# Performance work log

Measured on AMD Instinct MI355X. Metric: run time of the kernel, lower is better.

The kernel has to match this reference:

```python
import jax, jax.numpy as jnp
import numpy as np

B, T, C, H = 2, 2048, 1024, 16
HD = C // H  # 64

def setup_inputs() -> dict:
    key = jax.random.key(0)
    ks = jax.random.split(key, 9)
    s = 0.02
    return {
        "x": jax.random.normal(ks[0], (B, T, C), jnp.float32),
        "Wq": jax.random.normal(ks[1], (C, C), jnp.float32) * s,
        "bq": jax.random.normal(ks[2], (C,), jnp.float32) * s,
        "Wk": jax.random.normal(ks[3], (C, C), jnp.float32) * s,
        "bk": jax.random.normal(ks[4], (C,), jnp.float32) * s,
        "Wv": jax.random.normal(ks[5], (C, C), jnp.float32) * s,
        "bv": jax.random.normal(ks[6], (C,), jnp.float32) * s,
        "Wp": jax.random.normal(ks[7], (C, C), jnp.float32) * s,
        "bp": jax.random.normal(ks[8], (C,), jnp.float32) * s,
    }

def reference(x, Wq, bq, Wk, bk, Wv, bv, Wp, bp):
    Bb, Tt, Cc = x.shape
    hd = Cc // H
    # project and split heads: [B, H, T, hd]
    def heads(W, b):
        return (x @ W.T + b).reshape(Bb, Tt, H, hd).transpose(0, 2, 1, 3)
    q, k, v = heads(Wq, bq), heads(Wk, bk), heads(Wv, bv)
    scale = 1.0 / np.sqrt(hd).astype(np.float32)
    att = jnp.einsum('bhqd,bhkd->bhqk', q, k) * scale
    causal = jnp.tril(jnp.ones((Tt, Tt), bool))
    att = jnp.where(causal[None, None], att, -jnp.inf)
    att = jax.nn.softmax(att, axis=-1)
    y = jnp.einsum('bhqk,bhkd->bhqd', att, v)
    y = y.transpose(0, 2, 1, 3).reshape(Bb, Tt, Cc)
    return y @ Wp.T + bp
```

## Files before the change

kernel.cpp:

```cpp
#include <hip/hip_runtime.h>
#include <hip/hip_bf16.h>

#define Tsz 2048
#define Csz 1024
#define Hn 16

typedef short s8v __attribute__((ext_vector_type(8)));
typedef short s4v __attribute__((ext_vector_type(4)));
typedef float f4v __attribute__((ext_vector_type(4)));
typedef int   i4v __attribute__((ext_vector_type(4)));
typedef unsigned u2v __attribute__((ext_vector_type(2)));

#define QSCALE (0.125f * 1.44269504088896f)

__device__ __forceinline__ unsigned short bfr(float x) {
    return (unsigned short)((__builtin_bit_cast(unsigned, x) + 0x8000u) >> 16);
}
__device__ __forceinline__ unsigned pack2_rn(float a, float b) {
    const unsigned ua = __builtin_bit_cast(unsigned, a) + 0x8000u;
    const unsigned ub = __builtin_bit_cast(unsigned, b) + 0x8000u;
    return (ua >> 16) | (ub & 0xFFFF0000u);
}
__device__ __forceinline__ unsigned cvt2(float a, float b) {
    __hip_bfloat162 h = __float22bfloat162_rn(float2{a, b});
    unsigned r;
    __builtin_memcpy(&r, &h, 4);
    return r;
}

__device__ __forceinline__ void gload_lds(const void* g, void* l) {
    __builtin_amdgcn_global_load_lds(
        (const __attribute__((address_space(1))) void*)g,
        (__attribute__((address_space(3))) void*)l, 16, 0, 0);
}

__global__ void cvt6(const float* __restrict__ x, const float* __restrict__ wq,
                     const float* __restrict__ wk, const float* __restrict__ wv,
                     const float* __restrict__ wp,
                     short* __restrict__ xo, short* __restrict__ qo,
                     short* __restrict__ ko, short* __restrict__ vo,
                     short* __restrict__ po) {
    const int bx = blockIdx.x;
    const float* in; short* out; int ib;
    if (bx < 4096) { in = x; out = xo; ib = bx; }
    else {
        const int r = bx - 4096, w = r >> 10;
        ib = r & 1023;
        switch (w) {
            case 0: in = wq; out = qo; break;
            case 1: in = wk; out = ko; break;
            case 2: in = wv; out = vo; break;
            default: in = wp; out = po; break;
        }
    }
    const int i = ib * 1024 + threadIdx.x * 4;
    float4 v = *(const float4*)(in + i);
    int2 o;
    o.x = (int)pack2_rn(v.x, v.y);
    o.y = (int)pack2_rn(v.z, v.w);
    *(int2*)(out + i) = o;
}

__global__ __launch_bounds__(256, 3) void qkv_gemm(
    const short* __restrict__ X,
    const short* __restrict__ Wq, const short* __restrict__ Wk, const short* __restrict__ Wv,
    const float* __restrict__ bq, const float* __restrict__ bk, const float* __restrict__ bv,
    short* __restrict__ Qo, short* __restrict__ Ko, short* __restrict__ Vto)
{
    const int z = blockIdx.z;
    const short* W = (z == 0) ? Wq : (z == 1) ? Wk : Wv;
    const float* bias = (z == 0) ? bq : (z == 1) ? bk : bv;

    __shared__ __align__(16) short Ash[128 * 32];
    __shared__ __align__(16) short Bsh[128 * 32];
    __shared__ __align__(16) short TR[64 * 72];

    const int tid = threadIdx.x, lane = tid & 63, wave = tid >> 6;
    const int ln = lane & 15, hi = lane >> 4;
    const int m0 = blockIdx.x * 128, n0 = blockIdx.y * 128;
    const int wm = (wave >> 1) * 64, wn = (wave & 1) * 64;

    const short* Ag = X + (size_t)(m0 + (tid >> 2)) * Csz + (tid & 3) * 8;
    const short* Bg = W + (size_t)(n0 + (tid >> 2)) * Csz + (tid & 3) * 8;

    f4v acc[4][4];
    #pragma unroll
    for (int mt = 0; mt < 4; mt++)
        #pragma unroll
        for (int nt = 0; nt < 4; nt++)
            #pragma unroll
            for (int i = 0; i < 4; i++) acc[mt][nt][i] = 0.f;

    for (int k0 = 0; k0 < Csz; k0 += 32) {
        __syncthreads();
        gload_lds(Ag + k0, Ash + tid * 8);
        gload_lds(Ag + k0 + (size_t)64 * Csz, Ash + 2048 + tid * 8);
        gload_lds(Bg + k0, Bsh + tid * 8);
        gload_lds(Bg + k0 + (size_t)64 * Csz, Bsh + 2048 + tid * 8);
        __syncthreads();

        s8v af[4], bfr_[4];
        #pragma unroll
        for (int mt = 0; mt < 4; mt++)
            af[mt] = *(const s8v*)(Ash + (wm + mt * 16 + ln) * 32 + hi * 8);
        #pragma unroll
        for (int nt = 0; nt < 4; nt++)
            bfr_[nt] = *(const s8v*)(Bsh + (wn + nt * 16 + ln) * 32 + hi * 8);
        #pragma unroll
        for (int mt = 0; mt < 4; mt++)
            #pragma unroll
            for (int nt = 0; nt < 4; nt++)
                acc[mt][nt] = __builtin_amdgcn_mfma_f32_16x16x32_bf16(af[mt], bfr_[nt], acc[mt][nt], 0, 0, 0);
    }

    if (z == 2) {
        const int b = m0 >> 11, t0 = m0 & 2047;
        float bvv[4];
        #pragma unroll
        for (int nt = 0; nt < 4; nt++) bvv[nt] = bias[n0 + wn + nt * 16 + ln];
        #pragma unroll
        for (int ph = 0; ph < 4; ph++) {
            const int mh = ph >> 1, nh = ph & 1;
            __syncthreads();
            if ((wave >> 1) == mh && (wave & 1) == nh) {
                #pragma unroll
                for (int mt = 0; mt < 4; mt++)
                    #pragma unroll
                    for (int nt = 0; nt < 4; nt++) {
                        int2 pk;
                        pk.x = (int)pack2_rn(acc[mt][nt][0] + bvv[nt], acc[mt][nt][1] + bvv[nt]);
                        pk.y = (int)pack2_rn(acc[mt][nt][2] + bvv[nt], acc[mt][nt][3] + bvv[nt]);
                        *(int2*)(TR + (nt * 16 + ln) * 72 + mt * 16 + hi * 4) = pk;
                    }
            }
            __syncthreads();
            const int chl = tid >> 2, seg = tid & 3;
            const s8v r0 = *(const s8v*)(TR + chl * 72 + seg * 16);
            const s8v r1 = *(const s8v*)(TR + chl * 72 + seg * 16 + 8);
            short* dst = Vto + (size_t)(b * 1024 + n0 + nh * 64 + chl) * Tsz + t0 + mh * 64 + seg * 16;
            *(s8v*)(dst) = r0;
            *(s8v*)(dst + 8) = r1;
        }
        return;
    }

    const float scale = (z == 0) ? QSCALE : 1.0f;
    short* out = (z == 0) ? Qo : Ko;

    #pragma unroll
    for (int nt = 0; nt < 4; nt++) {
        const int col = n0 + wn + nt * 16 + ln;
        const float bvv = bias[col];
        #pragma unroll
        for (int mt = 0; mt < 4; mt++) {
            const int row0 = m0 + wm + mt * 16 + hi * 4;
            #pragma unroll
            for (int i = 0; i < 4; i++)
                out[(size_t)(row0 + i) * Csz + col] = (short)bfr((acc[mt][nt][i] + bvv) * scale);
        }
    }
}

__global__ __launch_bounds__(256, 2) void proj_gemm(
    const short* __restrict__ A, const short* __restrict__ W,
    const float* __restrict__ bias, float* __restrict__ out)
{
    __shared__ __align__(16) short Ash[128 * 32];
    __shared__ __align__(16) short Bsh[64 * 32];

    const int tid = threadIdx.x, lane = tid & 63, wave = tid >> 6;
    const int ln = lane & 15, hi = lane >> 4;
    const int m0 = blockIdx.x * 128, n0 = blockIdx.y * 64;
    const int wm = (wave >> 1) * 64, wn = (wave & 1) * 32;

    const short* Ag = A + (size_t)(m0 + (tid >> 2)) * Csz + (tid & 3) * 8;
    const short* Bg = W + (size_t)(n0 + (tid >> 2)) * Csz + (tid & 3) * 8;

    f4v acc[4][2];
    #pragma unroll
    for (int mt = 0; mt < 4; mt++)
        #pragma unroll
        for (int nt = 0; nt < 2; nt++)
            #pragma unroll
            for (int i = 0; i < 4; i++) acc[mt][nt][i] = 0.f;

    for (int k0 = 0; k0 < Csz; k0 += 32) {
        __syncthreads();
        gload_lds(Ag + k0, Ash + tid * 8);
        gload_lds(Ag + k0 + (size_t)64 * Csz, Ash + 2048 + tid * 8);
        gload_lds(Bg + k0, Bsh + tid * 8);
        __syncthreads();

        s8v af[4], bfr_[2];
        #pragma unroll
        for (int mt = 0; mt < 4; mt++)
            af[mt] = *(const s8v*)(Ash + (wm + mt * 16 + ln) * 32 + hi * 8);
        #pragma unroll
        for (int nt = 0; nt < 2; nt++)
            bfr_[nt] = *(const s8v*)(Bsh + (wn + nt * 16 + ln) * 32 + hi * 8);
        #pragma unroll
        for (int mt = 0; mt < 4; mt++)
            #pragma unroll
            for (int nt = 0; nt < 2; nt++)
                acc[mt][nt] = __builtin_amdgcn_mfma_f32_16x16x32_bf16(af[mt], bfr_[nt], acc[mt][nt], 0, 0, 0);
    }

    #pragma unroll
    for (int nt = 0; nt < 2; nt++) {
        const int col = n0 + wn + nt * 16 + ln;
        const float bvv = bias[col];
        #pragma unroll
        for (int mt = 0; mt < 4; mt++)
            #pragma unroll
            for (int i = 0; i < 4; i++)
                out[(size_t)(m0 + wm + mt * 16 + hi * 4 + i) * Csz + col] = acc[mt][nt][i] + bvv;
    }
}

__global__ __launch_bounds__(256, 2) void attn17(
    const short* __restrict__ Q, const short* __restrict__ Kg,
    const short* __restrict__ Vt, short* __restrict__ Y)
{
    __shared__ __align__(16) short SB[2][2][64 * 64];

    const int tid = threadIdx.x, lane = tid & 63, wave = tid >> 6;
    const int ln = lane & 15, hi = lane >> 4;

    const int n = blockIdx.x;
    const int j = n >> 8, n0 = n & 255;
    const int bh = n0 >> 3, ti = n0 & 7;
    const int t = j ? (15 - ti) : ti;
    const int qts_[2] = { t, 31 - t };
    const int nkb = 32 - t;

    const size_t base = (size_t)(bh >> 4) * Tsz * Csz + (size_t)(bh & 15) * 64;
    const size_t vtbase = (size_t)bh * 64 * Tsz;
    const int qrel = wave * 16 + ln;

    s8v qf[2][2];
    #pragma unroll
    for (int tt = 0; tt < 2; tt++)
        #pragma unroll
        for (int kk = 0; kk < 2; kk++)
            qf[tt][kk] = *(const s8v*)(Q + base + (size_t)(qts_[tt] * 64 + qrel) * Csz + kk * 32 + hi * 8);

    f4v o[2][4];
    f4v lacc[2];
    #pragma unroll
    for (int tt = 0; tt < 2; tt++) {
        #pragma unroll
        for (int i = 0; i < 4; i++) lacc[tt][i] = 0.f;
        #pragma unroll
        for (int dt = 0; dt < 4; dt++)
            #pragma unroll
            for (int i = 0; i < 4; i++) o[tt][dt][i] = 0.f;
    }

    const s8v ones8 = { (short)0x3F80, (short)0x3F80, (short)0x3F80, (short)0x3F80,
                        (short)0x3F80, (short)0x3F80, (short)0x3F80, (short)0x3F80 };

    const int sr = tid >> 3, scs = tid & 7;
    const int csw = (scs ^ (sr & 7)) * 8;
    const short* KsA = Kg + base + (size_t)sr * Csz + csw;
    const short* KsB = KsA + (size_t)32 * Csz;
    const short* VsA = Vt + vtbase + (size_t)sr * Tsz + csw;
    const short* VsB = VsA + (size_t)32 * Tsz;

    int foff[2][4];
    #pragma unroll
    for (int nt = 0; nt < 4; nt++)
        #pragma unroll
        for (int kk = 0; kk < 2; kk++)
            foff[kk][nt] = (nt * 16 + ln) * 64 + (((kk * 4 + hi) ^ (ln & 7)) * 8);

    #define STAGE(B, kb_) {                                      \
        const size_t ko_ = (size_t)(kb_) * 64;                   \
        gload_lds(KsA + ko_ * Csz, &SB[B][0][tid * 8]);          \
        gload_lds(KsB + ko_ * Csz, &SB[B][0][2048 + tid * 8]);   \
        gload_lds(VsA + ko_,       &SB[B][1][tid * 8]);          \
        gload_lds(VsB + ko_,       &SB[B][1][2048 + tid * 8]);   \
    }

    STAGE(0, 0);
    asm volatile("s_waitcnt vmcnt(0)" ::: "memory");
    __builtin_amdgcn_s_barrier();

    #define TILE(B0, B1, kb_) {                                                     \
        const bool st_ = (kb_) + 1 < nkb;                                           \
        if (st_) STAGE(B1, (kb_) + 1);                                              \
        s8v kf[2][4], vf[2][4];                                                     \
        for (int nt = 0; nt < 4; nt++) {                                            \
            kf[0][nt] = *(const s8v*)(&SB[B0][0][foff[0][nt]]);                     \
            kf[1][nt] = *(const s8v*)(&SB[B0][0][foff[1][nt]]);                     \
            vf[0][nt] = *(const s8v*)(&SB[B0][1][foff[0][nt]]);                     \
            vf[1][nt] = *(const s8v*)(&SB[B0][1][foff[1][nt]]);                     \
        }                                                                           \
        _Pragma("unroll")                                                           \
        for (int tt = 0; tt < 2; tt++) {                                            \
            if ((kb_) > qts_[tt]) continue;                       \
            f4v s[4];                                                               \
            for (int nt = 0; nt < 4; nt++) {                                        \
                for (int i = 0; i < 4; i++) s[nt][i] = 0.f;                         \
                s[nt] = __builtin_amdgcn_mfma_f32_16x16x32_bf16(kf[0][nt], qf[tt][0], s[nt], 0, 0, 0); \
                s[nt] = __builtin_amdgcn_mfma_f32_16x16x32_bf16(kf[1][nt], qf[tt][1], s[nt], 0, 0, 0); \
            }                                                                       \
            const bool dg_ = ((kb_) == qts_[tt]);                                   \
            unsigned pw[4][2];                                                      \
            for (int nt = 0; nt < 4; nt++) {                                        \
                float e0 = exp2f(s[nt][0]), e1 = exp2f(s[nt][1]);                   \
                float e2 = exp2f(s[nt][2]), e3 = exp2f(s[nt][3]);                   \
                if (dg_) {                                                          \
                    const int kr = nt * 16 + hi * 4;                                \
                    if (kr + 0 > qrel) e0 = 0.f;                                    \
                    if (kr + 1 > qrel) e1 = 0.f;                                    \
                    if (kr + 2 > qrel) e2 = 0.f;                                    \
                    if (kr + 3 > qrel) e3 = 0.f;                                    \
                }                                                                   \
                pw[nt][0] = cvt2(e0, e1);                                           \
                pw[nt][1] = cvt2(e2, e3);                                           \
            }                                                                       \
            u2v r0a = __builtin_amdgcn_permlane32_swap(pw[0][0], pw[1][0], false, false); \
            u2v r0b = __builtin_amdgcn_permlane16_swap(r0a[0], r0a[1], false, false); \
            u2v r1a = __builtin_amdgcn_permlane32_swap(pw[0][1], pw[1][1], false, false); \
            u2v r1b = __builtin_amdgcn_permlane16_swap(r1a[0], r1a[1], false, false); \
            u2v r2a = __builtin_amdgcn_permlane32_swap(pw[2][0], pw[3][0], false, false); \
            u2v r2b = __builtin_amdgcn_permlane16_swap(r2a[0], r2a[1], false, false); \
            u2v r3a = __builtin_amdgcn_permlane32_swap(pw[2][1], pw[3][1], false, false); \
            u2v r3b = __builtin_amdgcn_permlane16_swap(r3a[0], r3a[1], false, false); \
            i4v p0 = { (int)r0b[0], (int)r1b[0], (int)r0b[1], (int)r1b[1] };        \
            i4v p1 = { (int)r2b[0], (int)r3b[0], (int)r2b[1], (int)r3b[1] };        \
            const s8v pb0 = __builtin_bit_cast(s8v, p0);                            \
            const s8v pb1 = __builtin_bit_cast(s8v, p1);                            \
            for (int dt = 0; dt < 4; dt++) {                                        \
                o[tt][dt] = __builtin_amdgcn_mfma_f32_16x16x32_bf16(vf[0][dt], pb0, o[tt][dt], 0, 0, 0); \
                o[tt][dt] = __builtin_amdgcn_mfma_f32_16x16x32_bf16(vf[1][dt], pb1, o[tt][dt], 0, 0, 0); \
            }                                                                       \
            lacc[tt] = __builtin_amdgcn_mfma_f32_16x16x32_bf16(ones8, pb0, lacc[tt], 0, 0, 0); \
            lacc[tt] = __builtin_amdgcn_mfma_f32_16x16x32_bf16(ones8, pb1, lacc[tt], 0, 0, 0); \
        }                                                                           \
        if (st_) {                                                                  \
            asm volatile("s_waitcnt vmcnt(0)" ::: "memory");                        \
            __builtin_amdgcn_s_barrier();                                           \
        }                                                                           \
    }

    for (int kb = 0; kb < nkb; kb += 2) {
        TILE(0, 1, kb);
        if (kb + 1 < nkb) TILE(1, 0, kb + 1);
    }
    #undef TILE
    #undef STAGE

    #pragma unroll
    for (int tt = 0; tt < 2; tt++) {
        const float inv = 1.0f / lacc[tt][0];
        const int qrow = qts_[tt] * 64 + qrel;
        #pragma unroll
        for (int dt = 0; dt < 4; dt++) {
            int2 w;
            w.x = (int)cvt2(o[tt][dt][0] * inv, o[tt][dt][1] * inv);
            w.y = (int)cvt2(o[tt][dt][2] * inv, o[tt][dt][3] * inv);
            *(int2*)(Y + base + (size_t)qrow * Csz + dt * 16 + hi * 4) = w;
        }
    }
}

extern "C" void kernel_launch(void* const* d_in, const int* in_sizes, int n_in,
                              void* d_out, int out_size, void* d_ws, size_t ws_size,
                              hipStream_t stream) {
    const float* x  = (const float*)d_in[0];
    const float* Wq = (const float*)d_in[1];
    const float* bq = (const float*)d_in[2];
    const float* Wk = (const float*)d_in[3];
    const float* bk = (const float*)d_in[4];
    const float* Wv = (const float*)d_in[5];
    const float* bv = (const float*)d_in[6];
    const float* Wp = (const float*)d_in[7];
    const float* bp = (const float*)d_in[8];

    char* ws = (char*)d_ws;
    short* Xb  = (short*)(ws);
    short* Wqb = (short*)(ws + (8u  << 20));
    short* Wkb = (short*)(ws + (10u << 20));
    short* Wvb = (short*)(ws + (12u << 20));
    short* Wpb = (short*)(ws + (14u << 20));
    short* Qb  = (short*)(ws + (16u << 20));
    short* Kb  = (short*)(ws + (24u << 20));
    short* Vtb = (short*)(ws + (32u << 20));
    short* Yb  = (short*)(ws + (40u << 20));

    hipLaunchKernelGGL(cvt6, dim3(8192), dim3(256), 0, stream,
                       x, Wq, Wk, Wv, Wp, Xb, Wqb, Wkb, Wvb, Wpb);

    hipLaunchKernelGGL(qkv_gemm, dim3(32, 8, 3), dim3(256), 0, stream,
                       Xb, Wqb, Wkb, Wvb, bq, bk, bv, Qb, Kb, Vtb);

    hipLaunchKernelGGL(attn17, dim3(512), dim3(256), 0, stream, Qb, Kb, Vtb, Yb);

    hipLaunchKernelGGL(proj_gemm, dim3(32, 16), dim3(256), 0, stream, Yb, Wpb, bp, (float*)d_out);
}
```

Before: 178.8 us.

## Double-buffer LDS tiles in QKV and projection GEMMs to overlap loads with MFMA

The QKV and output-projection GEMM main loops now use two LDS buffers per operand. The next K-slice is prefetched with direct global-to-LDS loads while MFMAs run on the current slice, leaving one barrier per step instead of two. The aim is to hide global-load latency behind compute. In exchange, LDS use doubles, which may reduce occupancy for the 3-blocks-per-CU QKV kernel, and the hand-written vmcnt waits must cover the async LDS writes.

```diff
diff --git a/kernel.cpp b/kernel.cpp
--- a/kernel.cpp
+++ b/kernel.cpp
@@ -71,8 +71,8 @@
     const short* W = (z == 0) ? Wq : (z == 1) ? Wk : Wv;
     const float* bias = (z == 0) ? bq : (z == 1) ? bk : bv;
 
-    __shared__ __align__(16) short Ash[128 * 32];
-    __shared__ __align__(16) short Bsh[128 * 32];
+    __shared__ __align__(16) short Ash[2][128 * 32];
+    __shared__ __align__(16) short Bsh[2][128 * 32];
     __shared__ __align__(16) short TR[64 * 72];
 
     const int tid = threadIdx.x, lane = tid & 63, wave = tid >> 6;
@@ -91,27 +91,40 @@
             #pragma unroll
             for (int i = 0; i < 4; i++) acc[mt][nt][i] = 0.f;
 
-    for (int k0 = 0; k0 < Csz; k0 += 32) {
-        __syncthreads();
-        gload_lds(Ag + k0, Ash + tid * 8);
-        gload_lds(Ag + k0 + (size_t)64 * Csz, Ash + 2048 + tid * 8);
-        gload_lds(Bg + k0, Bsh + tid * 8);
-        gload_lds(Bg + k0 + (size_t)64 * Csz, Bsh + 2048 + tid * 8);
-        __syncthreads();
-
-        s8v af[4], bfr_[4];
-        #pragma unroll
-        for (int mt = 0; mt < 4; mt++)
-            af[mt] = *(const s8v*)(Ash + (wm + mt * 16 + ln) * 32 + hi * 8);
-        #pragma unroll
-        for (int nt = 0; nt < 4; nt++)
-            bfr_[nt] = *(const s8v*)(Bsh + (wn + nt * 16 + ln) * 32 + hi * 8);
-        #pragma unroll
-        for (int mt = 0; mt < 4; mt++)
-            #pragma unroll
-            for (int nt = 0; nt < 4; nt++)
-                acc[mt][nt] = __builtin_amdgcn_mfma_f32_16x16x32_bf16(af[mt], bfr_[nt], acc[mt][nt], 0, 0, 0);
-    }
+    #define QSTAGE(B, k0_) {                                              \
+        gload_lds(Ag + (k0_), Ash[B] + tid * 8);                          \
+        gload_lds(Ag + (k0_) + (size_t)64 * Csz, Ash[B] + 2048 + tid * 8);\
+        gload_lds(Bg + (k0_), Bsh[B] + tid * 8);                          \
+        gload_lds(Bg + (k0_) + (size_t)64 * Csz, Bsh[B] + 2048 + tid * 8);\
+    }
+
+    QSTAGE(0, 0);
+    asm volatile("s_waitcnt vmcnt(0)" ::: "memory");
+    __builtin_amdgcn_s_barrier();
+
+    #define QTILE(B, k0_) {                                                         \
+        const bool more_ = (k0_) + 32 < Csz;                                        \
+        if (more_) QSTAGE(B ^ 1, (k0_) + 32);                                       \
+        s8v af[4], bf_[4];                                                          \
+        for (int mt = 0; mt < 4; mt++)                                              \
+            af[mt] = *(const s8v*)(Ash[B] + (wm + mt * 16 + ln) * 32 + hi * 8);     \
+        for (int nt = 0; nt < 4; nt++)                                              \
+            bf_[nt] = *(const s8v*)(Bsh[B] + (wn + nt * 16 + ln) * 32 + hi * 8);    \
+        for (int mt = 0; mt < 4; mt++)                                              \
+            for (int nt = 0; nt < 4; nt++)                                          \
+                acc[mt][nt] = __builtin_amdgcn_mfma_f32_16x16x32_bf16(af[mt], bf_[nt], acc[mt][nt], 0, 0, 0); \
+        if (more_) {                                                                \
+            asm volatile("s_waitcnt vmcnt(0)" ::: "memory");                        \
+            __builtin_amdgcn_s_barrier();                                           \
+        }                                                                           \
+    }
+
+    for (int k0 = 0; k0 < Csz; k0 += 64) {
+        QTILE(0, k0);
+        QTILE(1, k0 + 32);
+    }
+    #undef QTILE
+    #undef QSTAGE
 
     if (z == 2) {
         const int b = m0 >> 11, t0 = m0 & 2047;
@@ -165,8 +178,8 @@
     const short* __restrict__ A, const short* __restrict__ W,
     const float* __restrict__ bias, float* __restrict__ out)
 {
-    __shared__ __align__(16) short Ash[128 * 32];
-    __shared__ __align__(16) short Bsh[64 * 32];
+    __shared__ __align__(16) short Ash[2][128 * 32];
+    __shared__ __align__(16) short Bsh[2][64 * 32];
 
     const int tid = threadIdx.x, lane = tid & 63, wave = tid >> 6;
     const int ln = lane & 15, hi = lane >> 4;
@@ -184,26 +197,39 @@
             #pragma unroll
             for (int i = 0; i < 4; i++) acc[mt][nt][i] = 0.f;
 
-    for (int k0 = 0; k0 < Csz; k0 += 32) {
-        __syncthreads();
-        gload_lds(Ag + k0, Ash + tid * 8);
-        gload_lds(Ag + k0 + (size_t)64 * Csz, Ash + 2048 + tid * 8);
-        gload_lds(Bg + k0, Bsh + tid * 8);
-        __syncthreads();
-
-        s8v af[4], bfr_[2];
-        #pragma unroll
-        for (int mt = 0; mt < 4; mt++)
-            af[mt] = *(const s8v*)(Ash + (wm + mt * 16 + ln) * 32 + hi * 8);
-        #pragma unroll
-        for (int nt = 0; nt < 2; nt++)
-            bfr_[nt] = *(const s8v*)(Bsh + (wn + nt * 16 + ln) * 32 + hi * 8);
-        #pragma unroll
-        for (int mt = 0; mt < 4; mt++)
-            #pragma unroll
-            for (int nt = 0; nt < 2; nt++)
-                acc[mt][nt] = __builtin_amdgcn_mfma_f32_16x16x32_bf16(af[mt], bfr_[nt], acc[mt][nt], 0, 0, 0);
-    }
+    #define PSTAGE(B, k0_) {                                              \
+        gload_lds(Ag + (k0_), Ash[B] + tid * 8);                          \
+        gload_lds(Ag + (k0_) + (size_t)64 * Csz, Ash[B] + 2048 + tid * 8);\
+        gload_lds(Bg + (k0_), Bsh[B] + tid * 8);                          \
+    }
+
+    PSTAGE(0, 0);
+    asm volatile("s_waitcnt vmcnt(0)" ::: "memory");
+    __builtin_amdgcn_s_barrier();
+
+    #define PTILE(B, k0_) {                                                         \
+        const bool more_ = (k0_) + 32 < Csz;                                        \
+        if (more_) PSTAGE(B ^ 1, (k0_) + 32);                                       \
+        s8v af[4], bf_[2];                                                          \
+        for (int mt = 0; mt < 4; mt++)                                              \
+            af[mt] = *(const s8v*)(Ash[B] + (wm + mt * 16 + ln) * 32 + hi * 8);     \
+        for (int nt = 0; nt < 2; nt++)                                              \
+            bf_[nt] = *(const s8v*)(Bsh[B] + (wn + nt * 16 + ln) * 32 + hi * 8);    \
+        for (int mt = 0; mt < 4; mt++)                                              \
+            for (int nt = 0; nt < 2; nt++)                                          \
+                acc[mt][nt] = __builtin_amdgcn_mfma_f32_16x16x32_bf16(af[mt], bf_[nt], acc[mt][nt], 0, 0, 0); \
+        if (more_) {                                                                \
+            asm volatile("s_waitcnt vmcnt(0)" ::: "memory");                        \
+            __builtin_amdgcn_s_barrier();                                           \
+        }                                                                           \
+    }
+
+    for (int k0 = 0; k0 < Csz; k0 += 64) {
+        PTILE(0, k0);
+        PTILE(1, k0 + 32);
+    }
+    #undef PTILE
+    #undef PSTAGE
 
     #pragma unroll
     for (int nt = 0; nt < 2; nt++) {
```

Measured after the change: 185.5 us. 3.8% more time.

## Double attention key-block size to 128 and share V fragments across query tiles

Applied to the files above, without the earlier changes.

The attention kernel now streams K/V in 128-key blocks instead of 64, halving the number of barrier/wait iterations, and adjusts the diagonal masking threshold for the larger block. V fragments are loaded from LDS once per k-slice and reused for both query tiles, instead of each tile holding its own copies. This raises LDS use to 64 KB per block and increases register pressure from 8 score tiles, which may hurt occupancy at 2 blocks per CU. It also computes some wasted masked work on diagonal blocks.

```diff
diff --git a/kernel.cpp b/kernel.cpp
--- a/kernel.cpp
+++ b/kernel.cpp
@@ -217,11 +217,11 @@
     }
 }
 
-__global__ __launch_bounds__(256, 2) void attn17(
+__global__ __launch_bounds__(256, 2) void attn19(
     const short* __restrict__ Q, const short* __restrict__ Kg,
     const short* __restrict__ Vt, short* __restrict__ Y)
 {
-    __shared__ __align__(16) short SB[2][2][64 * 64];
+    __shared__ __align__(16) short SB[2][2][128 * 64];
 
     const int tid = threadIdx.x, lane = tid & 63, wave = tid >> 6;
     const int ln = lane & 15, hi = lane >> 4;
@@ -231,11 +231,13 @@
     const int bh = n0 >> 3, ti = n0 & 7;
     const int t = j ? (15 - ti) : ti;
     const int qts_[2] = { t, 31 - t };
-    const int nkb = 32 - t;
+    const int dgk_[2] = { t >> 1, (31 - t) >> 1 };
+    const int nkb = dgk_[1] + 1;
 
     const size_t base = (size_t)(bh >> 4) * Tsz * Csz + (size_t)(bh & 15) * 64;
     const size_t vtbase = (size_t)bh * 64 * Tsz;
     const int qrel = wave * 16 + ln;
+    const int thr_[2] = { qrel + ((t & 1) << 6), qrel + (((31 - t) & 1) << 6) };
 
     s8v qf[2][2];
     #pragma unroll
@@ -260,25 +262,34 @@
                         (short)0x3F80, (short)0x3F80, (short)0x3F80, (short)0x3F80 };
 
     const int sr = tid >> 3, scs = tid & 7;
-    const int csw = (scs ^ (sr & 7)) * 8;
-    const short* KsA = Kg + base + (size_t)sr * Csz + csw;
-    const short* KsB = KsA + (size_t)32 * Csz;
-    const short* VsA = Vt + vtbase + (size_t)sr * Tsz + csw;
-    const short* VsB = VsA + (size_t)32 * Tsz;
-
-    int foff[2][4];
-    #pragma unroll
-    for (int nt = 0; nt < 4; nt++)
+    const short* KsA = Kg + base + (size_t)sr * Csz + (scs ^ (sr & 7)) * 8;
+    const int vr = tid >> 4, vscs = tid & 15;
+    const short* VsA = Vt + vtbase + (size_t)vr * Tsz + (vscs ^ (vr & 7)) * 8;
+
+    int fk[2][8];
+    #pragma unroll
+    for (int nt = 0; nt < 8; nt++)
         #pragma unroll
         for (int kk = 0; kk < 2; kk++)
-            foff[kk][nt] = (nt * 16 + ln) * 64 + (((kk * 4 + hi) ^ (ln & 7)) * 8);
-
-    #define STAGE(B, kb_) {                                      \
-        const size_t ko_ = (size_t)(kb_) * 64;                   \
-        gload_lds(KsA + ko_ * Csz, &SB[B][0][tid * 8]);          \
-        gload_lds(KsB + ko_ * Csz, &SB[B][0][2048 + tid * 8]);   \
-        gload_lds(VsA + ko_,       &SB[B][1][tid * 8]);          \
-        gload_lds(VsB + ko_,       &SB[B][1][2048 + tid * 8]);   \
+            fk[kk][nt] = (nt * 16 + ln) * 64 + (((kk * 4 + hi) ^ (ln & 7)) * 8);
+    int fv[4][4];
+    #pragma unroll
+    for (int dt = 0; dt < 4; dt++)
+        #pragma unroll
+        for (int kk = 0; kk < 4; kk++)
+            fv[kk][dt] = (dt * 16 + ln) * 128 + (((kk * 4 + hi) ^ (ln & 7)) * 8);
+
+    #define STAGE(B, kb_) {                                              \
+        const short* kp_ = KsA + (size_t)(kb_) * 128 * Csz;              \
+        const short* vp_ = VsA + (size_t)(kb_) * 128;                    \
+        gload_lds(kp_,                   &SB[B][0][tid * 8]);            \
+        gload_lds(kp_ + (size_t)32*Csz,  &SB[B][0][2048 + tid * 8]);     \
+        gload_lds(kp_ + (size_t)64*Csz,  &SB[B][0][4096 + tid * 8]);     \
+        gload_lds(kp_ + (size_t)96*Csz,  &SB[B][0][6144 + tid * 8]);     \
+        gload_lds(vp_,                   &SB[B][1][tid * 8]);            \
+        gload_lds(vp_ + (size_t)16*Tsz,  &SB[B][1][2048 + tid * 8]);     \
+        gload_lds(vp_ + (size_t)32*Tsz,  &SB[B][1][4096 + tid * 8]);     \
+        gload_lds(vp_ + (size_t)48*Tsz,  &SB[B][1][6144 + tid * 8]);     \
     }
 
     STAGE(0, 0);
@@ -288,55 +299,57 @@
     #define TILE(B0, B1, kb_) {                                                     \
         const bool st_ = (kb_) + 1 < nkb;                                           \
         if (st_) STAGE(B1, (kb_) + 1);                                              \
-        s8v kf[2][4], vf[2][4];                                                     \
-        for (int nt = 0; nt < 4; nt++) {                                            \
-            kf[0][nt] = *(const s8v*)(&SB[B0][0][foff[0][nt]]);                     \
-            kf[1][nt] = *(const s8v*)(&SB[B0][0][foff[1][nt]]);                     \
-            vf[0][nt] = *(const s8v*)(&SB[B0][1][foff[0][nt]]);                     \
-            vf[1][nt] = *(const s8v*)(&SB[B0][1][foff[1][nt]]);                     \
-        }                                                                           \
+        s8v pbt[2][4];                                                              \
+        bool act[2];                                                                \
+        act[0] = (kb_) <= dgk_[0];                                                  \
+        act[1] = (kb_) <= dgk_[1];                                                  \
         _Pragma("unroll")                                                           \
         for (int tt = 0; tt < 2; tt++) {                                            \
-            if ((kb_) > qts_[tt]) continue;                       \
-            f4v s[4];                                                               \
-            for (int nt = 0; nt < 4; nt++) {                                        \
+            if (!act[tt]) continue;                               \
+            f4v s[8];                                                               \
+            for (int nt = 0; nt < 8; nt++) {                                        \
+                const s8v k0_ = *(const s8v*)(&SB[B0][0][fk[0][nt]]);               \
+                const s8v k1_ = *(const s8v*)(&SB[B0][0][fk[1][nt]]);               \
                 for (int i = 0; i < 4; i++) s[nt][i] = 0.f;                         \
-                s[nt] = __builtin_amdgcn_mfma_f32_16x16x32_bf16(kf[0][nt], qf[tt][0], s[nt], 0, 0, 0); \
-                s[nt] = __builtin_amdgcn_mfma_f32_16x16x32_bf16(kf[1][nt], qf[tt][1], s[nt], 0, 0, 0); \
+                s[nt] = __builtin_amdgcn_mfma_f32_16x16x32_bf16(k0_, qf[tt][0], s[nt], 0, 0, 0); \
+                s[nt] = __builtin_amdgcn_mfma_f32_16x16x32_bf16(k1_, qf[tt][1], s[nt], 0, 0, 0); \
             }                                                                       \
-            const bool dg_ = ((kb_) == qts_[tt]);                                   \
-            unsigned pw[4][2];                                                      \
-            for (int nt = 0; nt < 4; nt++) {                                        \
+            const bool dg_ = ((kb_) == dgk_[tt]);                                   \
+            const int thr = thr_[tt];                                               \
+            unsigned pw[8][2];                                                      \
+            for (int nt = 0; nt < 8; nt++) {                                        \
                 float e0 = exp2f(s[nt][0]), e1 = exp2f(s[nt][1]);                   \
                 float e2 = exp2f(s[nt][2]), e3 = exp2f(s[nt][3]);                   \
                 if (dg_) {                                                          \
                     const int kr = nt * 16 + hi * 4;                                \
-                    if (kr + 0 > qrel) e0 = 0.f;                                    \
-                    if (kr + 1 > qrel) e1 = 0.f;                                    \
-                    if (kr + 2 > qrel) e2 = 0.f;                                    \
-                    if (kr + 3 > qrel) e3 = 0.f;                                    \
+                    if (kr + 0 > thr) e0 = 0.f;                                     \
+                    if (kr + 1 > thr) e1 = 0.f;                                     \
+                    if (kr + 2 > thr) e2 = 0.f;                                     \
+                    if (kr + 3 > thr) e3 = 0.f;                                     \
                 }                                                                   \
                 pw[nt][0] = cvt2(e0, e1);                                           \
                 pw[nt][1] = cvt2(e2, e3);                                           \
             }                                                                       \
-            u2v r0a = __builtin_amdgcn_permlane32_swap(pw[0][0], pw[1][0], false, false); \
-            u2v r0b = __builtin_amdgcn_permlane16_swap(r0a[0], r0a[1], false, false); \
-            u2v r1a = __builtin_amdgcn_permlane32_swap(pw[0][1], pw[1][1], false, false); \
-            u2v r1b = __builtin_amdgcn_permlane16_swap(r1a[0], r1a[1], false, false); \
-            u2v r2a = __builtin_amdgcn_permlane32_swap(pw[2][0], pw[3][0], false, false); \
-            u2v r2b = __builtin_amdgcn_permlane16_swap(r2a[0], r2a[1], false, false); \
-            u2v r3a = __builtin_amdgcn_permlane32_swap(pw[2][1], pw[3][1], false, false); \
-            u2v r3b = __builtin_amdgcn_permlane16_swap(r3a[0], r3a[1], false, false); \
-            i4v p0 = { (int)r0b[0], (int)r1b[0], (int)r0b[1], (int)r1b[1] };        \
-            i4v p1 = { (int)r2b[0], (int)r3b[0], (int)r2b[1], (int)r3b[1] };        \
-            const s8v pb0 = __builtin_bit_cast(s8v, p0);                            \
-            const s8v pb1 = __builtin_bit_cast(s8v, p1);                            \
-            for (int dt = 0; dt < 4; dt++) {                                        \
-                o[tt][dt] = __builtin_amdgcn_mfma_f32_16x16x32_bf16(vf[0][dt], pb0, o[tt][dt], 0, 0, 0); \
-                o[tt][dt] = __builtin_amdgcn_mfma_f32_16x16x32_bf16(vf[1][dt], pb1, o[tt][dt], 0, 0, 0); \
+            for (int e = 0; e < 4; e++) {                                           \
+                u2v ra = __builtin_amdgcn_permlane32_swap(pw[2*e][0], pw[2*e+1][0], false, false); \
+                u2v rb = __builtin_amdgcn_permlane16_swap(ra[0], ra[1], false, false); \
+                u2v rc = __builtin_amdgcn_permlane32_swap(pw[2*e][1], pw[2*e+1][1], false, false); \
+                u2v rd = __builtin_amdgcn_permlane16_swap(rc[0], rc[1], false, false); \
+                i4v pp = { (int)rb[0], (int)rd[0], (int)rb[1], (int)rd[1] };        \
+                pbt[tt][e] = __builtin_bit_cast(s8v, pp);                           \
             }                                                                       \
-            lacc[tt] = __builtin_amdgcn_mfma_f32_16x16x32_bf16(ones8, pb0, lacc[tt], 0, 0, 0); \
-            lacc[tt] = __builtin_amdgcn_mfma_f32_16x16x32_bf16(ones8, pb1, lacc[tt], 0, 0, 0); \
+        }                                                                           \
+        _Pragma("unroll")                                                           \
+        for (int kk = 0; kk < 4; kk++) {                                            \
+            s8v vfr[4];                                                             \
+            for (int dt = 0; dt < 4; dt++)                                          \
+                vfr[dt] = *(const s8v*)(&SB[B0][1][fv[kk][dt]]);                    \
+            for (int tt = 0; tt < 2; tt++) {                                        \
+                if (!act[tt]) continue;                                             \
+                for (int dt = 0; dt < 4; dt++)                                      \
+                    o[tt][dt] = __builtin_amdgcn_mfma_f32_16x16x32_bf16(vfr[dt], pbt[tt][kk], o[tt][dt], 0, 0, 0); \
+                lacc[tt] = __builtin_amdgcn_mfma_f32_16x16x32_bf16(ones8, pbt[tt][kk], lacc[tt], 0, 0, 0); \
+            }                                                                       \
         }                                                                           \
         if (st_) {                                                                  \
             asm volatile("s_waitcnt vmcnt(0)" ::: "memory");                        \
@@ -395,7 +408,7 @@
     hipLaunchKernelGGL(qkv_gemm, dim3(32, 8, 3), dim3(256), 0, stream,
                        Xb, Wqb, Wkb, Wvb, bq, bk, bv, Qb, Kb, Vtb);
 
-    hipLaunchKernelGGL(attn17, dim3(512), dim3(256), 0, stream, Qb, Kb, Vtb, Yb);
+    hipLaunchKernelGGL(attn19, dim3(512), dim3(256), 0, stream, Qb, Kb, Vtb, Yb);
 
     hipLaunchKernelGGL(proj_gemm, dim3(32, 16), dim3(256), 0, stream, Yb, Wpb, bp, (float*)d_out);
 }
```

New measurement: 184.4 us. +3.2%, slower.
